# Kernel tuning notes

Hardware: AMD Instinct MI355X
Metric: run time of the kernel (lower is better)

## Reference

```python
import jax, jax.numpy as jnp
import numpy as np

B, T, M = 32, 14, 2048
Q_DIM, KV_DIM, H = 768, 1024, 12
HD = Q_DIM // H
FF = 4 * Q_DIM
EPS = 1e-5


def layer_norm(x, g, b):
    mu = jnp.mean(x, axis=-1, keepdims=True)
    var = jnp.var(x, axis=-1, keepdims=True)
    return (x - mu) / jnp.sqrt(var + EPS) * g + b


def setup_inputs() -> dict:
    key = jax.random.key(0)
    ks = jax.random.split(key, 12)
    s = 0.02
    return {
        "expert_tokens": jax.random.normal(ks[0], (B, T, Q_DIM), jnp.float32),
        "key_value_embeddings": jax.random.normal(ks[1], (B, M, KV_DIM), jnp.float32),
        # per-expert-token query projections (stacked W_Q_list)
        "WQ": jax.random.normal(ks[2], (T, Q_DIM, Q_DIM), jnp.float32) * s,
        "bQ": jnp.zeros((T, Q_DIM), jnp.float32),
        "WK": jax.random.normal(ks[3], (KV_DIM, Q_DIM), jnp.float32) * s,
        "bK": jnp.zeros((Q_DIM,), jnp.float32),
        "WV": jax.random.normal(ks[4], (KV_DIM, Q_DIM), jnp.float32) * s,
        "bV": jnp.zeros((Q_DIM,), jnp.float32),
        "W1": jax.random.normal(ks[5], (Q_DIM, FF), jnp.float32) * s,
        "b1": jnp.zeros((FF,), jnp.float32),
        "W2": jax.random.normal(ks[6], (FF, Q_DIM), jnp.float32) * s,
        "b2": jnp.zeros((Q_DIM,), jnp.float32),
        "g1": jnp.ones((Q_DIM,), jnp.float32),
        "be1": jnp.zeros((Q_DIM,), jnp.float32),
        "g2": jnp.ones((Q_DIM,), jnp.float32),
        "be2": jnp.zeros((Q_DIM,), jnp.float32),
    }


def reference(expert_tokens, key_value_embeddings, WQ, bQ, WK, bK, WV, bV,
              W1, b1, W2, b2, g1, be1, g2, be2):
    b_, t_, e_ = expert_tokens.shape
    m_ = key_value_embeddings.shape[1]
    # Batched grouped projection: distinct W_Q per expert token (replaces the python loop)
    Q = (jnp.einsum('bte,teq->btq', expert_tokens, WQ) + bQ).reshape(b_, t_, H, HD)
    K = (key_value_embeddings @ WK + bK).reshape(b_, m_, H, HD)
    V = (key_value_embeddings @ WV + bV).reshape(b_, m_, H, HD)
    scale = jnp.sqrt(jnp.asarray(HD, jnp.float32))
    scores = jnp.einsum('bthd,bmhd->bthm', Q, K) / scale
    attn_w = jax.nn.softmax(scores, axis=-1)  # [B,T,H,M]; dropout is identity at eval
    attn_out = jnp.einsum('bthm,bmhd->bthd', attn_w, V).reshape(b_, t_, e_)
    x = layer_norm(expert_tokens + attn_out, g1, be1)
    ff = jnp.maximum(x @ W1 + b1, 0.0) @ W2 + b2
    out = layer_norm(x + ff, g2, be2)
    return out, attn_w
```

## Files before the change

kernel.cpp:

```cpp
#include <hip/hip_runtime.h>
#include <cstdint>
#include <cstddef>

#define BBATCH 32
#define TT 14
#define MM 2048
#define QD 768
#define NHEAD 12
#define HD 64
#define FFD 3072
#define KVD 1024

typedef short bf16x8 __attribute__((ext_vector_type(8)));
typedef float f32x4 __attribute__((ext_vector_type(4)));

__device__ __forceinline__ uint16_t f2b(float f) {
  union { float f; uint32_t u; } v; v.f = f;
  uint32_t r = v.u + 0x7fffu + ((v.u >> 16) & 1u);
  return (uint16_t)(r >> 16);
}
__device__ __forceinline__ float b2f(uint16_t b) {
  union { uint32_t u; float f; } v; v.u = ((uint32_t)b) << 16; return v.f;
}

__device__ __forceinline__ void glds16(const void* g, void* l) {
  __builtin_amdgcn_global_load_lds(
      (const __attribute__((address_space(1))) void*)g,
      (__attribute__((address_space(3))) void*)l, 16, 0, 0);
}

__global__ void k_cast8(const float4* __restrict__ in, uint4* __restrict__ out) {
  int i = blockIdx.x * blockDim.x + threadIdx.x;
  float4 a = in[2 * i], b = in[2 * i + 1];
  uint4 o;
  o.x = (uint32_t)f2b(a.x) | ((uint32_t)f2b(a.y) << 16);
  o.y = (uint32_t)f2b(a.z) | ((uint32_t)f2b(a.w) << 16);
  o.z = (uint32_t)f2b(b.x) | ((uint32_t)f2b(b.y) << 16);
  o.w = (uint32_t)f2b(b.z) | ((uint32_t)f2b(b.w) << 16);
  out[i] = o;
}

__global__ void k_transpose_bf16(const float* __restrict__ in, uint16_t* __restrict__ out,
                                 int R, int C) {
  __shared__ float tile[32][33];
  int bz = blockIdx.z;
  int c0 = blockIdx.x * 32, r0 = blockIdx.y * 32;
  int tx = threadIdx.x & 31, ty = threadIdx.x >> 5;
  const float* inb = in + (size_t)bz * R * C;
  uint16_t* outb = out + (size_t)bz * R * C;
#pragma unroll
  for (int rr = 0; rr < 32; rr += 8)
    tile[ty + rr][tx] = inb[(size_t)(r0 + ty + rr) * C + c0 + tx];
  __syncthreads();
#pragma unroll
  for (int rr = 0; rr < 32; rr += 8)
    outb[(size_t)(c0 + ty + rr) * R + r0 + tx] = f2b(tile[tx][ty + rr]);
}

__global__ void k_bias_concat(const float* __restrict__ bK, const float* __restrict__ bV,
                              float* __restrict__ out) {
  int i = blockIdx.x * 256 + threadIdx.x;
  out[i] = (i < QD) ? bK[i] : bV[i - QD];
}

__global__ __launch_bounds__(256) void k_gemm_kv(
    const uint16_t* __restrict__ A, const uint16_t* __restrict__ Bt,
    const float* __restrict__ bias, uint16_t* __restrict__ Kh, uint16_t* __restrict__ Vt) {
  __shared__ __align__(16) uint16_t As[3 * 4096];
  __shared__ __align__(16) uint16_t Bs[3 * 4096];
  const int K = KVD;
  int tid = threadIdx.x;
  int w = tid >> 6, l = tid & 63;

  int wgid = blockIdx.y * 12 + blockIdx.x;
  int swz = (wgid & 7) * 768 + (wgid >> 3);
  int bx = swz % 12, by = swz / 12;
  int m0 = by * 128, n0 = bx * 128;
  int wm = (w >> 1) * 64, wn = (w & 1) * 64;

  f32x4 zero4 = {0.f, 0.f, 0.f, 0.f};
  f32x4 acc[4][4];
#pragma unroll
  for (int i = 0; i < 4; i++)
#pragma unroll
    for (int j = 0; j < 4; j++) acc[i][j] = zero4;

  int sr = tid >> 2;
  int sc = (tid & 3) * 8;
  const uint16_t* gA0 = A + (size_t)(m0 + sr) * K + sc;
  const uint16_t* gA1 = A + (size_t)(m0 + 64 + sr) * K + sc;
  const uint16_t* gB0 = Bt + (size_t)(n0 + sr) * K + sc;
  const uint16_t* gB1 = Bt + (size_t)(n0 + 64 + sr) * K + sc;

  int lm = l & 15, q = l >> 4;

  auto stage = [&](int buf, int kt) {
    uint16_t* a = As + buf * 4096 + w * 512;
    uint16_t* b = Bs + buf * 4096 + w * 512;
    glds16(gA0 + kt, a);
    glds16(gA1 + kt, a + 2048);
    glds16(gB0 + kt, b);
    glds16(gB1 + kt, b + 2048);
  };
  auto compute = [&](int buf) {
    const uint16_t* as = As + buf * 4096;
    const uint16_t* bs = Bs + buf * 4096;
    bf16x8 af[4], bfv[4];
#pragma unroll
    for (int i = 0; i < 4; i++) {
      af[i] = *(const bf16x8*)&as[(wm + i * 16 + lm) * 32 + q * 8];
      bfv[i] = *(const bf16x8*)&bs[(wn + i * 16 + lm) * 32 + q * 8];
    }
#pragma unroll
    for (int i = 0; i < 4; i++)
#pragma unroll
      for (int j = 0; j < 4; j++)
        acc[i][j] = __builtin_amdgcn_mfma_f32_16x16x32_bf16(af[i], bfv[j], acc[i][j], 0, 0, 0);
  };

  const int NT = K / 32;
  stage(0, 0);
  stage(1, 32);
  int cur = 0;
  for (int t = 0; t < NT - 1; ++t) {
    asm volatile("s_waitcnt vmcnt(4)" ::: "memory");
    __builtin_amdgcn_s_barrier();
    if (t + 2 < NT) {
      int sb = cur + 2; if (sb >= 3) sb -= 3;
      stage(sb, (t + 2) * 32);
    }
    compute(cur);
    cur = (cur == 2) ? 0 : cur + 1;
  }
  asm volatile("s_waitcnt vmcnt(0)" ::: "memory");
  __builtin_amdgcn_s_barrier();
  compute(cur);

#pragma unroll
  for (int j = 0; j < 4; j++) {
    int col = n0 + wn + j * 16 + lm;
    float bc = bias[col];
    bool isV = col >= QD;
    int c2 = isV ? col - QD : col;
    int h = c2 >> 6, d = c2 & 63;
#pragma unroll
    for (int i = 0; i < 4; i++) {
      int rowb = m0 + wm + i * 16 + q * 4;
#pragma unroll
      for (int r = 0; r < 4; r++) {
        int row = rowb + r;
        int b = row >> 11, m = row & 2047;
        float v = acc[i][j][r] + bc;
        if (isV)
          Vt[((((size_t)b * NHEAD + h) * HD) + d) * MM + m] = f2b(v);
        else
          Kh[(((size_t)b * NHEAD + h) * MM + m) * HD + d] = f2b(v);
      }
    }
  }
}

template <bool RELU, bool OUTF32>
__global__ __launch_bounds__(256) void k_gemm64(
    const uint16_t* __restrict__ A, const uint16_t* __restrict__ Bt,
    const float* __restrict__ bias, void* __restrict__ Cv, int K, int N) {
  __shared__ __align__(16) uint16_t As[3 * 2048];
  __shared__ __align__(16) uint16_t Bs[3 * 2048];
  int tid = threadIdx.x;
  int w = tid >> 6, l = tid & 63;
  int m0 = blockIdx.y * 64, n0 = blockIdx.x * 64;
  int wm = (w >> 1) * 32, wn = (w & 1) * 32;
  f32x4 zero4 = {0.f, 0.f, 0.f, 0.f};
  f32x4 acc[2][2];
#pragma unroll
  for (int i = 0; i < 2; i++)
#pragma unroll
    for (int j = 0; j < 2; j++) acc[i][j] = zero4;

  int sr = tid >> 2, sc = (tid & 3) * 8;
  const uint16_t* gA = A + (size_t)(m0 + sr) * K + sc;
  const uint16_t* gB = Bt + (size_t)(n0 + sr) * K + sc;
  int lm = l & 15, q = l >> 4;

  auto stage = [&](int buf, int kt) {
    glds16(gA + kt, As + buf * 2048 + w * 512);
    glds16(gB + kt, Bs + buf * 2048 + w * 512);
  };
  auto compute = [&](int buf) {
    const uint16_t* as = As + buf * 2048;
    const uint16_t* bs = Bs + buf * 2048;
    bf16x8 af[2], bfv[2];
#pragma unroll
    for (int i = 0; i < 2; i++) {
      af[i] = *(const bf16x8*)&as[(wm + i * 16 + lm) * 32 + q * 8];
      bfv[i] = *(const bf16x8*)&bs[(wn + i * 16 + lm) * 32 + q * 8];
    }
#pragma unroll
    for (int i = 0; i < 2; i++)
#pragma unroll
      for (int j = 0; j < 2; j++)
        acc[i][j] = __builtin_amdgcn_mfma_f32_16x16x32_bf16(af[i], bfv[j], acc[i][j], 0, 0, 0);
  };

  const int NT = K / 32;
  stage(0, 0);
  stage(1, 32);
  int cur = 0;
  for (int t = 0; t < NT - 1; ++t) {
    asm volatile("s_waitcnt vmcnt(2)" ::: "memory");
    __builtin_amdgcn_s_barrier();
    if (t + 2 < NT) {
      int sb = cur + 2; if (sb >= 3) sb -= 3;
      stage(sb, (t + 2) * 32);
    }
    compute(cur);
    cur = (cur == 2) ? 0 : cur + 1;
  }
  asm volatile("s_waitcnt vmcnt(0)" ::: "memory");
  __builtin_amdgcn_s_barrier();
  compute(cur);

#pragma unroll
  for (int j = 0; j < 2; j++) {
    int col = n0 + wn + j * 16 + lm;
    float bc = bias[col];
#pragma unroll
    for (int i = 0; i < 2; i++) {
      int rowb = m0 + wm + i * 16 + q * 4;
#pragma unroll
      for (int r = 0; r < 4; r++) {
        float v = acc[i][j][r] + bc;
        if (RELU) v = fmaxf(v, 0.f);
        if (OUTF32)
          ((float*)Cv)[(size_t)(rowb + r) * N + col] = v;
        else
          ((uint16_t*)Cv)[(size_t)(rowb + r) * N + col] = f2b(v);
      }
    }
  }
}

__global__ __launch_bounds__(256) void k_gemm_q(
    const uint16_t* __restrict__ Xb, const uint16_t* __restrict__ WQt,
    const float* __restrict__ bQ, float* __restrict__ Q) {
  __shared__ __align__(16) uint16_t As[32 * 32];
  __shared__ __align__(16) uint16_t Bs[64 * 32];
  int tid = threadIdx.x;
  int w = tid >> 6, l = tid & 63;
  int t = blockIdx.y, n0 = blockIdx.x * 64;
  const uint16_t* Wt = WQt + (size_t)t * QD * QD;
  f32x4 zero4 = {0.f, 0.f, 0.f, 0.f};
  f32x4 acc[2] = {zero4, zero4};
  int sr = tid >> 2, sc = (tid & 3) * 8;
  const uint16_t* gA = Xb + ((size_t)(sr * TT + t)) * QD + sc;
  const uint16_t* gB = Wt + (size_t)(n0 + sr) * QD + sc;
  int lm = l & 15, q = l >> 4;
  for (int kt = 0; kt < QD; kt += 32) {
    __syncthreads();
    if (tid < 128) glds16(gA + kt, As + w * 512);
    glds16(gB + kt, Bs + w * 512);
    __syncthreads();
    bf16x8 bfv = *(const bf16x8*)&Bs[(w * 16 + lm) * 32 + q * 8];
#pragma unroll
    for (int i = 0; i < 2; i++) {
      bf16x8 af = *(const bf16x8*)&As[(i * 16 + lm) * 32 + q * 8];
      acc[i] = __builtin_amdgcn_mfma_f32_16x16x32_bf16(af, bfv, acc[i], 0, 0, 0);
    }
  }
  int col = n0 + w * 16 + lm;
  float bc = bQ[t * QD + col];
#pragma unroll
  for (int i = 0; i < 2; i++) {
    int b0 = i * 16 + q * 4;
#pragma unroll
    for (int r = 0; r < 4; r++) {
      int b = b0 + r;
      Q[((size_t)(b * TT + t)) * QD + col] = acc[i][r] + bc;
    }
  }
}

__global__ __launch_bounds__(256) void k_scores(
    const float* __restrict__ Q,
    const uint16_t* __restrict__ Kh,
    float* __restrict__ AW) {
  __shared__ __align__(16) float Qs[7][64];
  __shared__ float redv[4];
  int tid = threadIdx.x;
  int tg = blockIdx.x, h = blockIdx.y, b = blockIdx.z;
  int t0 = tg * 7;
  for (int i = tid; i < 7 * 64; i += 256) {
    int t = i >> 6, d = i & 63;
    Qs[t][d] = Q[((size_t)(b * TT + t0 + t)) * QD + h * HD + d] * 0.125f;
  }
  __syncthreads();
  float acc[7][8];
#pragma unroll
  for (int t = 0; t < 7; t++)
#pragma unroll
    for (int c = 0; c < 8; c++) acc[t][c] = 0.f;

  const uint16_t* kb = Kh + ((size_t)(b * NHEAD + h)) * MM * HD;
  for (int c = 0; c < 8; c++) {
    const uint16_t* kr = kb + (size_t)(c * 256 + tid) * HD;
#pragma unroll
    for (int dv = 0; dv < 8; dv++) {
      uint4 u = *(const uint4*)(kr + dv * 8);
      float kf[8];
      kf[0] = __uint_as_float(u.x << 16); kf[1] = __uint_as_float(u.x & 0xffff0000u);
      kf[2] = __uint_as_float(u.y << 16); kf[3] = __uint_as_float(u.y & 0xffff0000u);
      kf[4] = __uint_as_float(u.z << 16); kf[5] = __uint_as_float(u.z & 0xffff0000u);
      kf[6] = __uint_as_float(u.w << 16); kf[7] = __uint_as_float(u.w & 0xffff0000u);
#pragma unroll
      for (int t = 0; t < 7; t++) {
        float4 qa = *(const float4*)&Qs[t][dv * 8];
        float4 qb = *(const float4*)&Qs[t][dv * 8 + 4];
        float s = acc[t][c];
        s = fmaf(kf[0], qa.x, s); s = fmaf(kf[1], qa.y, s);
        s = fmaf(kf[2], qa.z, s); s = fmaf(kf[3], qa.w, s);
        s = fmaf(kf[4], qb.x, s); s = fmaf(kf[5], qb.y, s);
        s = fmaf(kf[6], qb.z, s); s = fmaf(kf[7], qb.w, s);
        acc[t][c] = s;
      }
    }
  }
  int lane = tid & 63, w = tid >> 6;
#pragma unroll
  for (int t = 0; t < 7; t++) {
    float mx = acc[t][0];
#pragma unroll
    for (int c = 1; c < 8; c++) mx = fmaxf(mx, acc[t][c]);
#pragma unroll
    for (int o = 32; o > 0; o >>= 1) mx = fmaxf(mx, __shfl_xor(mx, o));
    if (lane == 0) redv[w] = mx;
    __syncthreads();
    mx = fmaxf(fmaxf(redv[0], redv[1]), fmaxf(redv[2], redv[3]));
    __syncthreads();
    float s = 0.f;
#pragma unroll
    for (int c = 0; c < 8; c++) {
      float e = __expf(acc[t][c] - mx);
      acc[t][c] = e;
      s += e;
    }
#pragma unroll
    for (int o = 32; o > 0; o >>= 1) s += __shfl_xor(s, o);
    if (lane == 0) redv[w] = s;
    __syncthreads();
    s = redv[0] + redv[1] + redv[2] + redv[3];
    __syncthreads();
    float inv = 1.f / s;
    size_t rowb = ((size_t)((b * TT + t0 + t) * NHEAD + h)) * MM;
#pragma unroll
    for (int c = 0; c < 8; c++) AW[rowb + c * 256 + tid] = acc[t][c] * inv;
  }
}

__global__ __launch_bounds__(256) void k_attnout(
    const float* __restrict__ AW, const uint16_t* __restrict__ Vt,
    float* __restrict__ AO) {
  int tid = threadIdx.x;
  int h = blockIdx.x, b = blockIdx.y;
  int d = tid & 63, tg = tid >> 6;
  const uint16_t* vr = Vt + (((size_t)(b * NHEAD + h)) * HD + d) * MM;
  const float* pb = AW + ((size_t)(b * TT * NHEAD + h)) * MM;
  float acc[4] = {0.f, 0.f, 0.f, 0.f};
#pragma unroll 2
  for (int mc = 0; mc < MM; mc += 8) {
    uint4 u = *(const uint4*)(vr + mc);
    float vf[8];
    vf[0] = __uint_as_float(u.x << 16); vf[1] = __uint_as_float(u.x & 0xffff0000u);
    vf[2] = __uint_as_float(u.y << 16); vf[3] = __uint_as_float(u.y & 0xffff0000u);
    vf[4] = __uint_as_float(u.z << 16); vf[5] = __uint_as_float(u.z & 0xffff0000u);
    vf[6] = __uint_as_float(u.w << 16); vf[7] = __uint_as_float(u.w & 0xffff0000u);
#pragma unroll
    for (int i = 0; i < 4; i++) {
      int t = tg * 4 + i;
      if (t < TT) {
        const float* pr = pb + (size_t)t * NHEAD * MM + mc;
        float4 p0 = *(const float4*)pr;
        float4 p1 = *(const float4*)(pr + 4);
        float s = acc[i];
        s = fmaf(vf[0], p0.x, s); s = fmaf(vf[1], p0.y, s);
        s = fmaf(vf[2], p0.z, s); s = fmaf(vf[3], p0.w, s);
        s = fmaf(vf[4], p1.x, s); s = fmaf(vf[5], p1.y, s);
        s = fmaf(vf[6], p1.z, s); s = fmaf(vf[7], p1.w, s);
        acc[i] = s;
      }
    }
  }
#pragma unroll
  for (int i = 0; i < 4; i++) {
    int t = tg * 4 + i;
    if (t < TT) AO[((size_t)(b * TT + t)) * QD + h * HD + d] = acc[i];
  }
}

__global__ __launch_bounds__(256) void k_add_ln(
    const float* __restrict__ X, const float* __restrict__ Y,
    const float* __restrict__ g, const float* __restrict__ be,
    float* __restrict__ outF, uint16_t* __restrict__ outB) {
  __shared__ float redS[4], redQ[4];
  int r = blockIdx.x, tid = threadIdx.x;
  size_t base = (size_t)r * QD;
  float e[3];
  float s = 0.f, sq = 0.f;
#pragma unroll
  for (int j = 0; j < 3; j++) {
    float v = X[base + tid + j * 256] + Y[base + tid + j * 256];
    e[j] = v; s += v; sq += v * v;
  }
#pragma unroll
  for (int o = 32; o > 0; o >>= 1) { s += __shfl_xor(s, o); sq += __shfl_xor(sq, o); }
  if ((tid & 63) == 0) { redS[tid >> 6] = s; redQ[tid >> 6] = sq; }
  __syncthreads();
  s = redS[0] + redS[1] + redS[2] + redS[3];
  sq = redQ[0] + redQ[1] + redQ[2] + redQ[3];
  float mu = s * (1.f / QD);
  float var = sq * (1.f / QD) - mu * mu;
  float rstd = rsqrtf(var + 1e-5f);
#pragma unroll
  for (int j = 0; j < 3; j++) {
    int i = tid + j * 256;
    float v = (e[j] - mu) * rstd * g[i] + be[i];
    outF[base + i] = v;
    if (outB) outB[base + i] = f2b(v);
  }
}

extern "C" void kernel_launch(void* const* d_in, const int* in_sizes, int n_in,
                              void* d_out, int out_size, void* d_ws, size_t ws_size,
                              hipStream_t stream) {
  const float* tok = (const float*)d_in[0];
  const float* kve = (const float*)d_in[1];
  const float* WQ  = (const float*)d_in[2];
  const float* bQ  = (const float*)d_in[3];
  const float* WK  = (const float*)d_in[4];
  const float* bK  = (const float*)d_in[5];
  const float* WV  = (const float*)d_in[6];
  const float* bV  = (const float*)d_in[7];
  const float* W1  = (const float*)d_in[8];
  const float* b1  = (const float*)d_in[9];
  const float* W2  = (const float*)d_in[10];
  const float* b2  = (const float*)d_in[11];
  const float* g1  = (const float*)d_in[12];
  const float* be1 = (const float*)d_in[13];
  const float* g2  = (const float*)d_in[14];
  const float* be2 = (const float*)d_in[15];

  float* outp = (float*)d_out;
  float* AW = outp + 448 * 768;

  char* p = (char*)d_ws;
  auto nxt = [&](size_t bytes) -> char* {
    char* r = p;
    p += (bytes + 255) & ~(size_t)255;
    return r;
  };
  uint16_t* Abf   = (uint16_t*)nxt((size_t)67108864 * 2);
  uint16_t* Kh    = (uint16_t*)nxt((size_t)50331648 * 2);
  uint16_t* Vt    = (uint16_t*)nxt((size_t)50331648 * 2);
  uint16_t* Wkvt  = (uint16_t*)nxt((size_t)1572864 * 2);
  uint16_t* WQt   = (uint16_t*)nxt((size_t)8257536 * 2);
  uint16_t* W1t   = (uint16_t*)nxt((size_t)2359296 * 2);
  uint16_t* W2t   = (uint16_t*)nxt((size_t)2359296 * 2);
  uint16_t* xtokb = (uint16_t*)nxt((size_t)344064 * 2);
  float* biaskv   = (float*)nxt(1536 * 4);
  float* Qws      = (float*)nxt((size_t)344064 * 4);
  float* AOws     = (float*)nxt((size_t)344064 * 4);
  float* xws      = (float*)nxt((size_t)344064 * 4);
  uint16_t* xbf   = (uint16_t*)nxt((size_t)344064 * 2);
  uint16_t* h1bf  = (uint16_t*)nxt((size_t)1376256 * 2);
  float* yws      = (float*)nxt((size_t)344064 * 4);

  k_cast8<<<dim3(32768), dim3(256), 0, stream>>>((const float4*)kve, (uint4*)Abf);
  k_cast8<<<dim3(168), dim3(256), 0, stream>>>((const float4*)tok, (uint4*)xtokb);
  k_transpose_bf16<<<dim3(24, 32, 1), dim3(256), 0, stream>>>(WK, Wkvt, 1024, 768);
  k_transpose_bf16<<<dim3(24, 32, 1), dim3(256), 0, stream>>>(WV, Wkvt + (size_t)768 * 1024, 1024, 768);
  k_transpose_bf16<<<dim3(24, 24, 14), dim3(256), 0, stream>>>(WQ, WQt, 768, 768);
  k_transpose_bf16<<<dim3(96, 24, 1), dim3(256), 0, stream>>>(W1, W1t, 768, 3072);
  k_transpose_bf16<<<dim3(24, 96, 1), dim3(256), 0, stream>>>(W2, W2t, 3072, 768);
  k_bias_concat<<<dim3(6), dim3(256), 0, stream>>>(bK, bV, biaskv);

  k_gemm_kv<<<dim3(12, 512), dim3(256), 0, stream>>>(Abf, Wkvt, biaskv, Kh, Vt);

  k_gemm_q<<<dim3(12, 14), dim3(256), 0, stream>>>(xtokb, WQt, bQ, Qws);

  k_scores<<<dim3(2, 12, 32), dim3(256), 0, stream>>>(Qws, Kh, AW);

  k_attnout<<<dim3(12, 32), dim3(256), 0, stream>>>(AW, Vt, AOws);

  k_add_ln<<<dim3(448), dim3(256), 0, stream>>>(tok, AOws, g1, be1, xws, xbf);

  k_gemm64<true, false><<<dim3(48, 7), dim3(256), 0, stream>>>(xbf, W1t, b1, (void*)h1bf, 768, 3072);
  k_gemm64<false, true><<<dim3(12, 7), dim3(256), 0, stream>>>(h1bf, W2t, b2, (void*)yws, 3072, 768);

  k_add_ln<<<dim3(448), dim3(256), 0, stream>>>(xws, yws, g2, be2, outp, (uint16_t*)nullptr);
}
```

Baseline: 1.404 ms.

## Widen KV GEMM tile to 128x256 and XOR-swizzle LDS layout in GEMMs

The K/V projection GEMM now computes a 128x256 output tile per workgroup instead of 128x128, with each wave holding a 64x128 accumulator. This halves the re-reads of the A operand and the number of workgroups, and it adjusts the grid, the swizzle and the vmcnt wait to match. Separately, all three GEMMs use an XOR swizzle on the 16-byte chunk position inside each LDS row, applied both when staging global loads and when reading fragments, to reduce LDS bank conflicts. The larger tile raises register and LDS use, which may limit occupancy despite the launch bound of 2.

```diff
diff --git a/kernel.cpp b/kernel.cpp
--- a/kernel.cpp
+++ b/kernel.cpp
@@ -63,58 +63,64 @@
   out[i] = (i < QD) ? bK[i] : bV[i - QD];
 }
 
-__global__ __launch_bounds__(256) void k_gemm_kv(
+__global__ __launch_bounds__(256, 2) void k_gemm_kv(
     const uint16_t* __restrict__ A, const uint16_t* __restrict__ Bt,
     const float* __restrict__ bias, uint16_t* __restrict__ Kh, uint16_t* __restrict__ Vt) {
   __shared__ __align__(16) uint16_t As[3 * 4096];
-  __shared__ __align__(16) uint16_t Bs[3 * 4096];
+  __shared__ __align__(16) uint16_t Bs[3 * 8192];
   const int K = KVD;
   int tid = threadIdx.x;
   int w = tid >> 6, l = tid & 63;
 
-  int wgid = blockIdx.y * 12 + blockIdx.x;
-  int swz = (wgid & 7) * 768 + (wgid >> 3);
-  int bx = swz % 12, by = swz / 12;
-  int m0 = by * 128, n0 = bx * 128;
-  int wm = (w >> 1) * 64, wn = (w & 1) * 64;
+  int wgid = blockIdx.y * 6 + blockIdx.x;
+  int swz = (wgid & 7) * 384 + (wgid >> 3);
+  int bx = swz % 6, by = swz / 6;
+  int m0 = by * 128, n0 = bx * 256;
+  int wm = (w >> 1) * 64, wn = (w & 1) * 128;
 
   f32x4 zero4 = {0.f, 0.f, 0.f, 0.f};
-  f32x4 acc[4][4];
+  f32x4 acc[4][8];
 #pragma unroll
   for (int i = 0; i < 4; i++)
 #pragma unroll
-    for (int j = 0; j < 4; j++) acc[i][j] = zero4;
+    for (int j = 0; j < 8; j++) acc[i][j] = zero4;
 
   int sr = tid >> 2;
-  int sc = (tid & 3) * 8;
-  const uint16_t* gA0 = A + (size_t)(m0 + sr) * K + sc;
-  const uint16_t* gA1 = A + (size_t)(m0 + 64 + sr) * K + sc;
-  const uint16_t* gB0 = Bt + (size_t)(n0 + sr) * K + sc;
-  const uint16_t* gB1 = Bt + (size_t)(n0 + 64 + sr) * K + sc;
+  int xs8 = (((tid & 3) ^ ((tid >> 3) & 3))) * 8;
+  const uint16_t* gA0 = A + (size_t)(m0 + sr) * K + xs8;
+  const uint16_t* gA1 = A + (size_t)(m0 + 64 + sr) * K + xs8;
+  const uint16_t* gB0 = Bt + (size_t)(n0 + sr) * K + xs8;
+  const uint16_t* gB1 = Bt + (size_t)(n0 + 64 + sr) * K + xs8;
+  const uint16_t* gB2 = Bt + (size_t)(n0 + 128 + sr) * K + xs8;
+  const uint16_t* gB3 = Bt + (size_t)(n0 + 192 + sr) * K + xs8;
 
   int lm = l & 15, q = l >> 4;
+  int qp = (q ^ ((lm >> 1) & 3)) * 8;
 
   auto stage = [&](int buf, int kt) {
     uint16_t* a = As + buf * 4096 + w * 512;
-    uint16_t* b = Bs + buf * 4096 + w * 512;
+    uint16_t* b = Bs + buf * 8192 + w * 512;
     glds16(gA0 + kt, a);
     glds16(gA1 + kt, a + 2048);
     glds16(gB0 + kt, b);
     glds16(gB1 + kt, b + 2048);
+    glds16(gB2 + kt, b + 4096);
+    glds16(gB3 + kt, b + 6144);
   };
   auto compute = [&](int buf) {
     const uint16_t* as = As + buf * 4096;
-    const uint16_t* bs = Bs + buf * 4096;
-    bf16x8 af[4], bfv[4];
-#pragma unroll
-    for (int i = 0; i < 4; i++) {
-      af[i] = *(const bf16x8*)&as[(wm + i * 16 + lm) * 32 + q * 8];
-      bfv[i] = *(const bf16x8*)&bs[(wn + i * 16 + lm) * 32 + q * 8];
-    }
+    const uint16_t* bs = Bs + buf * 8192;
+    bf16x8 af[4], bfv[8];
 #pragma unroll
     for (int i = 0; i < 4; i++)
-#pragma unroll
-      for (int j = 0; j < 4; j++)
+      af[i] = *(const bf16x8*)&as[(wm + i * 16 + lm) * 32 + qp];
+#pragma unroll
+    for (int j = 0; j < 8; j++)
+      bfv[j] = *(const bf16x8*)&bs[(wn + j * 16 + lm) * 32 + qp];
+#pragma unroll
+    for (int i = 0; i < 4; i++)
+#pragma unroll
+      for (int j = 0; j < 8; j++)
         acc[i][j] = __builtin_amdgcn_mfma_f32_16x16x32_bf16(af[i], bfv[j], acc[i][j], 0, 0, 0);
   };
 
@@ -123,7 +129,7 @@
   stage(1, 32);
   int cur = 0;
   for (int t = 0; t < NT - 1; ++t) {
-    asm volatile("s_waitcnt vmcnt(4)" ::: "memory");
+    asm volatile("s_waitcnt vmcnt(6)" ::: "memory");
     __builtin_amdgcn_s_barrier();
     if (t + 2 < NT) {
       int sb = cur + 2; if (sb >= 3) sb -= 3;
@@ -137,7 +143,7 @@
   compute(cur);
 
 #pragma unroll
-  for (int j = 0; j < 4; j++) {
+  for (int j = 0; j < 8; j++) {
     int col = n0 + wn + j * 16 + lm;
     float bc = bias[col];
     bool isV = col >= QD;
@@ -177,10 +183,12 @@
 #pragma unroll
     for (int j = 0; j < 2; j++) acc[i][j] = zero4;
 
-  int sr = tid >> 2, sc = (tid & 3) * 8;
-  const uint16_t* gA = A + (size_t)(m0 + sr) * K + sc;
-  const uint16_t* gB = Bt + (size_t)(n0 + sr) * K + sc;
+  int sr = tid >> 2;
+  int xs8 = (((tid & 3) ^ ((tid >> 3) & 3))) * 8;
+  const uint16_t* gA = A + (size_t)(m0 + sr) * K + xs8;
+  const uint16_t* gB = Bt + (size_t)(n0 + sr) * K + xs8;
   int lm = l & 15, q = l >> 4;
+  int qp = (q ^ ((lm >> 1) & 3)) * 8;
 
   auto stage = [&](int buf, int kt) {
     glds16(gA + kt, As + buf * 2048 + w * 512);
@@ -192,8 +200,8 @@
     bf16x8 af[2], bfv[2];
 #pragma unroll
     for (int i = 0; i < 2; i++) {
-      af[i] = *(const bf16x8*)&as[(wm + i * 16 + lm) * 32 + q * 8];
-      bfv[i] = *(const bf16x8*)&bs[(wn + i * 16 + lm) * 32 + q * 8];
+      af[i] = *(const bf16x8*)&as[(wm + i * 16 + lm) * 32 + qp];
+      bfv[i] = *(const bf16x8*)&bs[(wn + i * 16 + lm) * 32 + qp];
     }
 #pragma unroll
     for (int i = 0; i < 2; i++)
@@ -251,19 +259,21 @@
   const uint16_t* Wt = WQt + (size_t)t * QD * QD;
   f32x4 zero4 = {0.f, 0.f, 0.f, 0.f};
   f32x4 acc[2] = {zero4, zero4};
-  int sr = tid >> 2, sc = (tid & 3) * 8;
-  const uint16_t* gA = Xb + ((size_t)(sr * TT + t)) * QD + sc;
-  const uint16_t* gB = Wt + (size_t)(n0 + sr) * QD + sc;
+  int sr = tid >> 2;
+  int xs8 = (((tid & 3) ^ ((tid >> 3) & 3))) * 8;
+  const uint16_t* gA = Xb + ((size_t)(sr * TT + t)) * QD + xs8;
+  const uint16_t* gB = Wt + (size_t)(n0 + sr) * QD + xs8;
   int lm = l & 15, q = l >> 4;
+  int qp = (q ^ ((lm >> 1) & 3)) * 8;
   for (int kt = 0; kt < QD; kt += 32) {
     __syncthreads();
     if (tid < 128) glds16(gA + kt, As + w * 512);
     glds16(gB + kt, Bs + w * 512);
     __syncthreads();
-    bf16x8 bfv = *(const bf16x8*)&Bs[(w * 16 + lm) * 32 + q * 8];
+    bf16x8 bfv = *(const bf16x8*)&Bs[(w * 16 + lm) * 32 + qp];
 #pragma unroll
     for (int i = 0; i < 2; i++) {
-      bf16x8 af = *(const bf16x8*)&As[(i * 16 + lm) * 32 + q * 8];
+      bf16x8 af = *(const bf16x8*)&As[(i * 16 + lm) * 32 + qp];
       acc[i] = __builtin_amdgcn_mfma_f32_16x16x32_bf16(af, bfv, acc[i], 0, 0, 0);
     }
   }
@@ -482,7 +492,7 @@
   k_transpose_bf16<<<dim3(24, 96, 1), dim3(256), 0, stream>>>(W2, W2t, 3072, 768);
   k_bias_concat<<<dim3(6), dim3(256), 0, stream>>>(bK, bV, biaskv);
 
-  k_gemm_kv<<<dim3(12, 512), dim3(256), 0, stream>>>(Abf, Wkvt, biaskv, Kh, Vt);
+  k_gemm_kv<<<dim3(6, 512), dim3(256), 0, stream>>>(Abf, Wkvt, biaskv, Kh, Vt);
 
   k_gemm_q<<<dim3(12, 14), dim3(256), 0, stream>>>(xtokb, WQt, bQ, Qws);
 
```

Result: no change. 1.403 ms (-0.0%).
